# Performance work log

Measured on AMD Instinct MI355X. Metric: run time of the kernel, lower is better.

The kernel has to match this reference:

```python
import jax, jax.numpy as jnp
import numpy as np

N_ATOMS = 50000
N_INT = 800000  # interactions (i,j pairs)
N_IN = 128
NFM = 128
LOG2 = float(np.log(2.0))


def ssp(a):
    # shifted softplus: log(0.5*exp(x) + 0.5) = softplus(x) - log(2)
    return jax.nn.softplus(a) - LOG2


def setup_inputs() -> dict:
    key = jax.random.key(0)
    ks = jax.random.split(key, 12)
    s = 1.0 / np.sqrt(NFM)
    inp = {
        "x": jax.random.normal(ks[0], (N_ATOMS, NFM), dtype=jnp.float32),
        "dijk": jax.random.normal(ks[1], (N_INT, N_IN), dtype=jnp.float32),
        "idx_j": jax.random.randint(ks[2], (N_INT,), 0, N_ATOMS),
        "seg_i": jnp.sort(jax.random.randint(ks[3], (N_INT,), 0, N_ATOMS)),
        "seg_j": jnp.arange(N_INT),
        "seg_i_sum": jnp.ones((N_ATOMS,), dtype=jnp.int64 if jax.config.jax_enable_x64 else jnp.int32),
        # filternet params
        "W_f1": jax.random.normal(ks[4], (N_IN, NFM), dtype=jnp.float32) * s,
        "b_f1": jnp.zeros((NFM,), dtype=jnp.float32),
        "W_f2": jax.random.normal(ks[5], (NFM, NFM), dtype=jnp.float32) * s,
        "b_f2": jnp.zeros((NFM,), dtype=jnp.float32),
        # cfconv params
        "W_in2fac": jax.random.normal(ks[6], (NFM, NFM), dtype=jnp.float32) * s,
        "W_fac2out": jax.random.normal(ks[7], (NFM, NFM), dtype=jnp.float32) * s,
        "b_fac2out": jnp.zeros((NFM,), dtype=jnp.float32),
        # output dense params
        "W_dense": jax.random.normal(ks[8], (NFM, NFM), dtype=jnp.float32) * s,
        "b_dense": jnp.zeros((NFM,), dtype=jnp.float32),
    }
    return inp


def reference(x, dijk, idx_j, seg_i, seg_j, seg_i_sum,
              W_f1, b_f1, W_f2, b_f2,
              W_in2fac, W_fac2out, b_fac2out,
              W_dense, b_dense):
    n_atoms = x.shape[0]
    n_int = idx_j.shape[0]
    # CFnetFilter: two shifted-softplus dense layers over triples, pool -> per-interaction filters
    h = ssp(dijk @ W_f1 + b_f1)                                   # [T, nFM]
    w_ijk = ssp(h @ W_f2 + b_f2)                                  # [T, nFM]
    w_ij = jax.ops.segment_sum(w_ijk, seg_j, num_segments=n_int)  # [E, nFM]
    # CFConv: in2fac dense, gather neighbor features, filter-multiply, segment-sum pool, fac2out dense
    f = x @ W_in2fac                                              # [N, nFM]
    f_j = f[idx_j]                                                # gather -> [E, nFM]
    wf = w_ij * f_j                                               # [E, nFM]
    conv = jax.ops.segment_sum(wf, seg_i, num_segments=n_atoms)   # [N, nFM]
    c = ssp(conv @ W_fac2out + b_fac2out)                         # [N, nFM]
    # output dense (no activation) + residual
    v = c @ W_dense + b_dense                                     # [N, nFM]
    y = x + v
    return (y, v)
```

## Files before the change

kernel.cpp:

```cpp
#include <hip/hip_runtime.h>
#include <hip/hip_bf16.h>
#include <stdint.h>

#define NATOMS 50000
#define NINT   800000
#define NFM    128
#define VOFF   (NATOMS*NFM)
#define NBLK   (NINT/256)
#define CVROWS 512
#define CVBLK  ((NINT + CVROWS - 1)/CVROWS)

typedef __bf16 bf16x8 __attribute__((ext_vector_type(8)));
typedef float  f32x4  __attribute__((ext_vector_type(4)));
typedef unsigned short u16;
typedef u16 u16x8 __attribute__((ext_vector_type(8)));
typedef u16 u16x4 __attribute__((ext_vector_type(4)));

__device__ __forceinline__ u16 f2b(float f){
  __bf16 h = (__bf16)f;
  return __builtin_bit_cast(u16, h);
}
__device__ __forceinline__ float b2f(u16 v){
  return (float)__builtin_bit_cast(__bf16, v);
}

__device__ __forceinline__ float sspf(float x){
  float t = exp2f(x * 1.44269504088896f);
  return 0.69314718055995f * (log2f(1.0f + t) - 1.0f);
}

__global__ void zero_k(float4* __restrict__ p, int n4){
  int i = blockIdx.x * blockDim.x + threadIdx.x;
  int stride = gridDim.x * blockDim.x;
  float4 z = make_float4(0.f, 0.f, 0.f, 0.f);
  for (; i < n4; i += stride) p[i] = z;
}

__global__ void prep_weights_k(const float* __restrict__ w0, const float* __restrict__ w1,
                               const float* __restrict__ w2, const float* __restrict__ w3,
                               const float* __restrict__ w4, u16* __restrict__ wt){
  const float* srcs[5] = {w0, w1, w2, w3, w4};
  const float* src = srcs[blockIdx.x];
  u16* dst = wt + (size_t)blockIdx.x * NFM * NFM;
  for (int i = threadIdx.x; i < NFM*NFM; i += blockDim.x){
    int n = i >> 7, k = i & 127;
    dst[i] = f2b(src[k*NFM + n]);
  }
}

__device__ __forceinline__ void stage_inp(u16* lsA, const float* __restrict__ src,
                                          int base_row, int n_total, int t){
  #pragma unroll
  for (int pp = 0; pp < 8; ++pp){
    int id  = pp*512 + t;
    int row = id >> 4, c = id & 15;
    int grow = base_row + row;
    float4 v0 = make_float4(0.f,0.f,0.f,0.f), v1 = v0;
    if (grow < n_total){
      const float4* gp = reinterpret_cast<const float4*>(src + (size_t)grow*NFM + c*8);
      v0 = gp[0]; v1 = gp[1];
    }
    u16x8 pk;
    pk[0]=f2b(v0.x); pk[1]=f2b(v0.y); pk[2]=f2b(v0.z); pk[3]=f2b(v0.w);
    pk[4]=f2b(v1.x); pk[5]=f2b(v1.y); pk[6]=f2b(v1.z); pk[7]=f2b(v1.w);
    int byte = row*256 + ((c*16) ^ ((row & 7) << 4));
    *reinterpret_cast<u16x8*>(reinterpret_cast<char*>(lsA) + byte) = pk;
  }
}

__device__ __forceinline__ void stage_w(u16* lsW, const u16* __restrict__ wt, int t){
  #pragma unroll
  for (int pp = 0; pp < 4; ++pp){
    int id = pp*512 + t;
    int n = id >> 4, c = id & 15;
    u16x8 v = *reinterpret_cast<const u16x8*>(wt + n*NFM + c*8);
    int byte = n*256 + ((c*16) ^ ((n & 7) << 4));
    *reinterpret_cast<u16x8*>(reinterpret_cast<char*>(lsW) + byte) = v;
  }
}

__device__ __forceinline__ void gemm_tile(const u16* lsA, const u16* lsW,
                                          int wrow, int l15, int lk, f32x4 acc[2][8]){
  #pragma unroll
  for (int ks = 0; ks < 4; ++ks){
    int kb2 = (ks*32 + lk*8) * 2;
    int r0 = wrow + l15, r1 = wrow + 16 + l15;
    bf16x8 a0 = *reinterpret_cast<const bf16x8*>(reinterpret_cast<const char*>(lsA) + r0*256 + (kb2 ^ ((r0 & 7) << 4)));
    bf16x8 a1 = *reinterpret_cast<const bf16x8*>(reinterpret_cast<const char*>(lsA) + r1*256 + (kb2 ^ ((r1 & 7) << 4)));
    #pragma unroll
    for (int ni = 0; ni < 8; ++ni){
      int n = ni*16 + l15;
      bf16x8 b = *reinterpret_cast<const bf16x8*>(reinterpret_cast<const char*>(lsW) + n*256 + (kb2 ^ ((n & 7) << 4)));
      acc[0][ni] = __builtin_amdgcn_mfma_f32_16x16x32_bf16(a0, b, acc[0][ni], 0, 0, 0);
      acc[1][ni] = __builtin_amdgcn_mfma_f32_16x16x32_bf16(a1, b, acc[1][ni], 0, 0, 0);
    }
  }
}

__global__ __launch_bounds__(512, 2) void in2fac_k(const float* __restrict__ x,
                                                   const u16* __restrict__ wt,
                                                   u16* __restrict__ f_g){
  __shared__ u16 lsA[256*128];
  __shared__ u16 lsW[128*128];
  int t = threadIdx.x;
  int B0 = blockIdx.x * 256;
  stage_inp(lsA, x, B0, NATOMS, t);
  stage_w(lsW, wt, t);
  __syncthreads();
  int wid = t >> 6, lane = t & 63, l15 = lane & 15, lk = lane >> 4;
  int wrow = wid * 32;
  f32x4 acc[2][8] = {};
  gemm_tile(lsA, lsW, wrow, l15, lk, acc);
  #pragma unroll
  for (int mi = 0; mi < 2; ++mi)
    #pragma unroll
    for (int ni = 0; ni < 8; ++ni)
      #pragma unroll
      for (int j = 0; j < 4; ++j){
        int grow = B0 + wrow + mi*16 + lk*4 + j;
        if (grow < NATOMS) f_g[(size_t)grow*NFM + ni*16 + l15] = f2b(acc[mi][ni][j]);
      }
}

__global__ __launch_bounds__(512) __attribute__((amdgpu_waves_per_eu(4, 4)))
void filter_k(const float* __restrict__ dijk,
              const float* __restrict__ b_f1, const float* __restrict__ b_f2,
              const u16* __restrict__ wt1, const u16* __restrict__ wt2,
              u16* __restrict__ w_g){
  __shared__ u16 lsW[2*128*128];
  __shared__ u16 lsS[8192];
  int t = threadIdx.x;
  int B0 = blockIdx.x * 256;
  int wid = t >> 6, lane = t & 63, l15 = lane & 15, lk = lane >> 4;

  f32x4 araw[16];
  {
    const float* abase = dijk + (size_t)(B0 + wid*32 + l15) * NFM;
    #pragma unroll
    for (int mi = 0; mi < 2; ++mi)
      #pragma unroll
      for (int ks = 0; ks < 4; ++ks){
        const f32x4* gp = reinterpret_cast<const f32x4*>(abase + mi*16*NFM + ks*32 + lk*8);
        araw[(mi*4+ks)*2+0] = __builtin_nontemporal_load(gp);
        araw[(mi*4+ks)*2+1] = __builtin_nontemporal_load(gp+1);
      }
  }

  stage_w(lsW, wt1, t);
  stage_w(lsW + 16384, wt2, t);

  float bias1[8], bias2[8];
  #pragma unroll
  for (int ni = 0; ni < 8; ++ni){ bias1[ni] = b_f1[ni*16 + l15]; bias2[ni] = b_f2[ni*16 + l15]; }

  bf16x8 aa[2][4];
  #pragma unroll
  for (int mi = 0; mi < 2; ++mi)
    #pragma unroll
    for (int ks = 0; ks < 4; ++ks){
      f32x4 v0 = araw[(mi*4+ks)*2], v1 = araw[(mi*4+ks)*2+1];
      u16x8 pk;
      pk[0]=f2b(v0[0]); pk[1]=f2b(v0[1]); pk[2]=f2b(v0[2]); pk[3]=f2b(v0[3]);
      pk[4]=f2b(v1[0]); pk[5]=f2b(v1[1]); pk[6]=f2b(v1[2]); pk[7]=f2b(v1[3]);
      aa[mi][ks] = __builtin_bit_cast(bf16x8, pk);
    }

  __syncthreads();

  char* wbase = reinterpret_cast<char*>(lsS) + wid*2048;
  const char* lsW1b = reinterpret_cast<const char*>(lsW);
  const char* lsW2b = reinterpret_cast<const char*>(lsW + 16384);

  #pragma unroll
  for (int mi = 0; mi < 2; ++mi){
    f32x4 acc[8] = {};
    #pragma unroll
    for (int ks = 0; ks < 4; ++ks){
      int kb2 = (ks*32 + lk*8) * 2;
      #pragma unroll
      for (int ni = 0; ni < 8; ++ni){
        int n = ni*16 + l15;
        bf16x8 b = *reinterpret_cast<const bf16x8*>(lsW1b + n*256 + (kb2 ^ ((n & 7) << 4)));
        acc[ni] = __builtin_amdgcn_mfma_f32_16x16x32_bf16(aa[mi][ks], b, acc[ni], 0, 0, 0);
      }
    }
    bf16x8 h[4];
    #pragma unroll
    for (int p = 0; p < 2; ++p){
      #pragma unroll
      for (int nn = 0; nn < 4; ++nn){
        int col = nn*16 + l15;
        #pragma unroll
        for (int j = 0; j < 4; ++j){
          int r = lk*4 + j;
          *reinterpret_cast<u16*>(wbase + r*128 + ((col*2) ^ ((r & 7) << 4))) = f2b(sspf(acc[p*4+nn][j] + bias1[p*4+nn]));
        }
      }
      #pragma unroll
      for (int ksl = 0; ksl < 2; ++ksl)
        h[p*2+ksl] = *reinterpret_cast<const bf16x8*>(wbase + l15*128 + ((ksl*64 + lk*16) ^ ((l15 & 7) << 4)));
    }
    #pragma unroll
    for (int p = 0; p < 2; ++p){
      f32x4 acc2[4] = {};
      #pragma unroll
      for (int ks = 0; ks < 4; ++ks){
        int kb2 = (ks*32 + lk*8) * 2;
        #pragma unroll
        for (int nn = 0; nn < 4; ++nn){
          int n = (p*4 + nn)*16 + l15;
          bf16x8 b = *reinterpret_cast<const bf16x8*>(lsW2b + n*256 + (kb2 ^ ((n & 7) << 4)));
          acc2[nn] = __builtin_amdgcn_mfma_f32_16x16x32_bf16(h[ks], b, acc2[nn], 0, 0, 0);
        }
      }
      #pragma unroll
      for (int nn = 0; nn < 4; ++nn){
        int col = nn*16 + l15;
        #pragma unroll
        for (int j = 0; j < 4; ++j){
          int r = lk*4 + j;
          *reinterpret_cast<u16*>(wbase + r*128 + ((col*2) ^ ((r & 7) << 4))) = f2b(sspf(acc2[nn][j] + bias2[p*4+nn]));
        }
      }
      int row16 = lane & 15, chunk = lane >> 4;
      u16x8 v0 = *reinterpret_cast<const u16x8*>(wbase + row16*128 + ((chunk*32) ^ ((row16 & 7) << 4)));
      u16x8 v1 = *reinterpret_cast<const u16x8*>(wbase + row16*128 + ((chunk*32 + 16) ^ ((row16 & 7) << 4)));
      u16* gdst = w_g + (size_t)(B0 + wid*32 + mi*16 + row16)*NFM + p*64 + chunk*16;
      *reinterpret_cast<u16x8*>(gdst)     = v0;
      *reinterpret_cast<u16x8*>(gdst + 8) = v1;
    }
  }
}

__global__ __launch_bounds__(512) void conv_k(const int* __restrict__ idx_j,
    const int* __restrict__ seg_i, const u16* __restrict__ f_g,
    const u16* __restrict__ w_g, float* __restrict__ conv){
  __shared__ int lsSeg[CVROWS];
  __shared__ int lsIdx[CVROWS];
  int t = threadIdx.x;
  int B0 = blockIdx.x * CVROWS;
  int navail = NINT - B0; if (navail > CVROWS) navail = CVROWS;
  if (t < navail){ lsSeg[t] = seg_i[B0 + t]; lsIdx[t] = idx_j[B0 + t]; }
  __syncthreads();
  int col = t & 127, q = t >> 7;
  int qs = q*128;
  if (qs >= navail) return;
  int qe = qs + 128; if (qe > navail) qe = navail;
  int prevseg = (qs > 0) ? lsSeg[qs-1] : (B0 > 0 ? seg_i[B0-1] : -1);
  int nextseg = (qe < navail) ? lsSeg[qe] : (B0 + qe < NINT ? seg_i[B0+qe] : -1);
  const u16* wtile = w_g + (size_t)B0*NFM;
  float s = 0.f;
  int cur = lsSeg[qs], rs = qs;
  for (int base = qs; base < qe; base += 16){
    float wbuf[16], fbuf[16];
    #pragma unroll
    for (int k = 0; k < 16; ++k){
      int r = base + k;
      wbuf[k] = b2f(wtile[(size_t)r*NFM + col]);
      fbuf[k] = b2f(f_g[(size_t)lsIdx[r]*NFM + col]);
    }
    #pragma unroll
    for (int k = 0; k < 16; ++k){
      int r = base + k;
      int sg = lsSeg[r];
      if (sg != cur){
        float* dp = conv + (size_t)cur*NFM + col;
        if (rs == qs && prevseg == cur) atomicAdd(dp, s); else *dp = s;
        cur = sg; rs = r; s = 0.f;
      }
      s = fmaf(wbuf[k], fbuf[k], s);
    }
  }
  float* dp = conv + (size_t)cur*NFM + col;
  if ((rs == qs && prevseg == cur) || nextseg == cur) atomicAdd(dp, s); else *dp = s;
}

__global__ __launch_bounds__(512, 2) void out_k(const float* __restrict__ conv,
    const float* __restrict__ x, const u16* __restrict__ wt3, const u16* __restrict__ wt4,
    const float* __restrict__ b3, const float* __restrict__ b4, float* __restrict__ out){
  __shared__ u16 lsA[256*128];
  __shared__ u16 lsW1[128*128];
  __shared__ u16 lsW2[128*128];
  int t = threadIdx.x;
  int B0 = blockIdx.x * 256;
  stage_inp(lsA, conv, B0, NATOMS, t);
  stage_w(lsW1, wt3, t);
  stage_w(lsW2, wt4, t);
  __syncthreads();
  int wid = t >> 6, lane = t & 63, l15 = lane & 15, lk = lane >> 4;
  int wrow = wid * 32;
  float bias3[8], bias4[8];
  #pragma unroll
  for (int ni = 0; ni < 8; ++ni){ bias3[ni] = b3[ni*16 + l15]; bias4[ni] = b4[ni*16 + l15]; }

  f32x4 acc1[2][8] = {};
  gemm_tile(lsA, lsW1, wrow, l15, lk, acc1);
  #pragma unroll
  for (int mi = 0; mi < 2; ++mi)
    #pragma unroll
    for (int ni = 0; ni < 8; ++ni)
      #pragma unroll
      for (int j = 0; j < 4; ++j){
        int row = wrow + mi*16 + lk*4 + j;
        int col = ni*16 + l15;
        u16 hb = f2b(sspf(acc1[mi][ni][j] + bias3[ni]));
        int byte = row*256 + ((col*2) ^ ((row & 7) << 4));
        *reinterpret_cast<u16*>(reinterpret_cast<char*>(lsA) + byte) = hb;
      }

  f32x4 acc2[2][8] = {};
  gemm_tile(lsA, lsW2, wrow, l15, lk, acc2);
  #pragma unroll
  for (int mi = 0; mi < 2; ++mi)
    #pragma unroll
    for (int ni = 0; ni < 8; ++ni)
      #pragma unroll
      for (int j = 0; j < 4; ++j){
        int grow = B0 + wrow + mi*16 + lk*4 + j;
        if (grow < NATOMS){
          int col = ni*16 + l15;
          float v = acc2[mi][ni][j] + bias4[ni];
          float yv = x[(size_t)grow*NFM + col] + v;
          out[(size_t)grow*NFM + col] = yv;
          out[(size_t)VOFF + (size_t)grow*NFM + col] = v;
        }
      }
}

extern "C" void kernel_launch(void* const* d_in, const int* in_sizes, int n_in,
                              void* d_out, int out_size, void* d_ws, size_t ws_size,
                              hipStream_t stream){
  const float* x        = (const float*)d_in[0];
  const float* dijk     = (const float*)d_in[1];
  const int*   idx_j    = (const int*)d_in[2];
  const int*   seg_i    = (const int*)d_in[3];
  const float* W_f1     = (const float*)d_in[6];
  const float* b_f1     = (const float*)d_in[7];
  const float* W_f2     = (const float*)d_in[8];
  const float* b_f2     = (const float*)d_in[9];
  const float* W_in2fac = (const float*)d_in[10];
  const float* W_fac2o  = (const float*)d_in[11];
  const float* b_fac2o  = (const float*)d_in[12];
  const float* W_dense  = (const float*)d_in[13];
  const float* b_dense  = (const float*)d_in[14];
  float* out = (float*)d_out;

  char* ws = (char*)d_ws;
  u16*   f_g  = (u16*)ws;
  float* conv = (float*)(ws + 12800000);
  u16*   wt   = (u16*)(ws + 38400000);
  u16*   w_g  = (u16*)(ws + 38600000);
  u16* wt1 = wt;
  u16* wt2 = wt + 16384;
  u16* wt5 = wt + 2*16384;
  u16* wt3 = wt + 3*16384;
  u16* wt4 = wt + 4*16384;

  prep_weights_k<<<5, 256, 0, stream>>>(W_f1, W_f2, W_in2fac, W_fac2o, W_dense, wt);
  zero_k<<<2048, 256, 0, stream>>>(reinterpret_cast<float4*>(conv), NATOMS*NFM/4);
  in2fac_k<<<(NATOMS + 255)/256, 512, 0, stream>>>(x, wt5, f_g);
  filter_k<<<NBLK, 512, 0, stream>>>(dijk, b_f1, b_f2, wt1, wt2, w_g);
  conv_k<<<CVBLK, 512, 0, stream>>>(idx_j, seg_i, f_g, w_g, conv);
  out_k<<<(NATOMS + 255)/256, 512, 0, stream>>>(conv, x, wt3, wt4, b_fac2o, b_dense, out);
}
```

Baseline: 303.1 us.

## Split filter and conv into two chunks to keep filter output cache-resident

Runs the filter and conv kernels in two row chunks, each writing and then reading a half-sized w_g buffer at offset zero. The intent is for the filter output to still be in the large last-level cache when conv reads it, cutting HBM round-trip traffic. The conv kernel gains per-row guards because a chunk can end partway through a 16-row group. The cost is two extra kernel launches, slightly more branching in conv, and a reduced-occupancy tail for each chunk.

```diff
diff --git a/kernel.cpp b/kernel.cpp
--- a/kernel.cpp
+++ b/kernel.cpp
@@ -6,15 +6,18 @@
 #define NINT   800000
 #define NFM    128
 #define VOFF   (NATOMS*NFM)
-#define NBLK   (NINT/256)
+#define F0BLK  1563
+#define F1BLK  1562
+#define C0ROWS (F0BLK*256)
+#define C1ROWS (F1BLK*256)
 #define CVROWS 512
-#define CVBLK  ((NINT + CVROWS - 1)/CVROWS)
+#define CV0BLK ((C0ROWS + CVROWS - 1)/CVROWS)
+#define CV1BLK ((C1ROWS + CVROWS - 1)/CVROWS)
 
 typedef __bf16 bf16x8 __attribute__((ext_vector_type(8)));
 typedef float  f32x4  __attribute__((ext_vector_type(4)));
 typedef unsigned short u16;
 typedef u16 u16x8 __attribute__((ext_vector_type(8)));
-typedef u16 u16x4 __attribute__((ext_vector_type(4)));
 
 __device__ __forceinline__ u16 f2b(float f){
   __bf16 h = (__bf16)f;
@@ -126,11 +129,11 @@
 void filter_k(const float* __restrict__ dijk,
               const float* __restrict__ b_f1, const float* __restrict__ b_f2,
               const u16* __restrict__ wt1, const u16* __restrict__ wt2,
-              u16* __restrict__ w_g){
+              u16* __restrict__ w_g, int C0){
   __shared__ u16 lsW[2*128*128];
   __shared__ u16 lsS[8192];
   int t = threadIdx.x;
-  int B0 = blockIdx.x * 256;
+  int B0 = C0 + blockIdx.x * 256;
   int wid = t >> 6, lane = t & 63, l15 = lane & 15, lk = lane >> 4;
 
   f32x4 araw[16];
@@ -225,7 +228,7 @@
       int row16 = lane & 15, chunk = lane >> 4;
       u16x8 v0 = *reinterpret_cast<const u16x8*>(wbase + row16*128 + ((chunk*32) ^ ((row16 & 7) << 4)));
       u16x8 v1 = *reinterpret_cast<const u16x8*>(wbase + row16*128 + ((chunk*32 + 16) ^ ((row16 & 7) << 4)));
-      u16* gdst = w_g + (size_t)(B0 + wid*32 + mi*16 + row16)*NFM + p*64 + chunk*16;
+      u16* gdst = w_g + (size_t)(blockIdx.x*256 + wid*32 + mi*16 + row16)*NFM + p*64 + chunk*16;
       *reinterpret_cast<u16x8*>(gdst)     = v0;
       *reinterpret_cast<u16x8*>(gdst + 8) = v1;
     }
@@ -234,12 +237,13 @@
 
 __global__ __launch_bounds__(512) void conv_k(const int* __restrict__ idx_j,
     const int* __restrict__ seg_i, const u16* __restrict__ f_g,
-    const u16* __restrict__ w_g, float* __restrict__ conv){
+    const u16* __restrict__ w_g, float* __restrict__ conv, int C0, int NROWS){
   __shared__ int lsSeg[CVROWS];
   __shared__ int lsIdx[CVROWS];
   int t = threadIdx.x;
-  int B0 = blockIdx.x * CVROWS;
-  int navail = NINT - B0; if (navail > CVROWS) navail = CVROWS;
+  int L0 = blockIdx.x * CVROWS;
+  int B0 = C0 + L0;
+  int navail = NROWS - L0; if (navail > CVROWS) navail = CVROWS;
   if (t < navail){ lsSeg[t] = seg_i[B0 + t]; lsIdx[t] = idx_j[B0 + t]; }
   __syncthreads();
   int col = t & 127, q = t >> 7;
@@ -248,27 +252,32 @@
   int qe = qs + 128; if (qe > navail) qe = navail;
   int prevseg = (qs > 0) ? lsSeg[qs-1] : (B0 > 0 ? seg_i[B0-1] : -1);
   int nextseg = (qe < navail) ? lsSeg[qe] : (B0 + qe < NINT ? seg_i[B0+qe] : -1);
-  const u16* wtile = w_g + (size_t)B0*NFM;
+  const u16* wtile = w_g + (size_t)L0*NFM;
   float s = 0.f;
   int cur = lsSeg[qs], rs = qs;
   for (int base = qs; base < qe; base += 16){
+    int bend = base + 16; if (bend > qe) bend = qe;
     float wbuf[16], fbuf[16];
     #pragma unroll
     for (int k = 0; k < 16; ++k){
       int r = base + k;
-      wbuf[k] = b2f(wtile[(size_t)r*NFM + col]);
-      fbuf[k] = b2f(f_g[(size_t)lsIdx[r]*NFM + col]);
+      if (r < bend){
+        wbuf[k] = b2f(wtile[(size_t)r*NFM + col]);
+        fbuf[k] = b2f(f_g[(size_t)lsIdx[r]*NFM + col]);
+      } else { wbuf[k] = 0.f; fbuf[k] = 0.f; }
     }
     #pragma unroll
     for (int k = 0; k < 16; ++k){
       int r = base + k;
-      int sg = lsSeg[r];
-      if (sg != cur){
-        float* dp = conv + (size_t)cur*NFM + col;
-        if (rs == qs && prevseg == cur) atomicAdd(dp, s); else *dp = s;
-        cur = sg; rs = r; s = 0.f;
-      }
-      s = fmaf(wbuf[k], fbuf[k], s);
+      if (r < bend){
+        int sg = lsSeg[r];
+        if (sg != cur){
+          float* dp = conv + (size_t)cur*NFM + col;
+          if (rs == qs && prevseg == cur) atomicAdd(dp, s); else *dp = s;
+          cur = sg; rs = r; s = 0.f;
+        }
+        s = fmaf(wbuf[k], fbuf[k], s);
+      }
     }
   }
   float* dp = conv + (size_t)cur*NFM + col;
@@ -359,7 +368,9 @@
   prep_weights_k<<<5, 256, 0, stream>>>(W_f1, W_f2, W_in2fac, W_fac2o, W_dense, wt);
   zero_k<<<2048, 256, 0, stream>>>(reinterpret_cast<float4*>(conv), NATOMS*NFM/4);
   in2fac_k<<<(NATOMS + 255)/256, 512, 0, stream>>>(x, wt5, f_g);
-  filter_k<<<NBLK, 512, 0, stream>>>(dijk, b_f1, b_f2, wt1, wt2, w_g);
-  conv_k<<<CVBLK, 512, 0, stream>>>(idx_j, seg_i, f_g, w_g, conv);
+  filter_k<<<F0BLK, 512, 0, stream>>>(dijk, b_f1, b_f2, wt1, wt2, w_g, 0);
+  conv_k<<<CV0BLK, 512, 0, stream>>>(idx_j, seg_i, f_g, w_g, conv, 0, C0ROWS);
+  filter_k<<<F1BLK, 512, 0, stream>>>(dijk, b_f1, b_f2, wt1, wt2, w_g, C0ROWS);
+  conv_k<<<CV1BLK, 512, 0, stream>>>(idx_j, seg_i, f_g, w_g, conv, C0ROWS, C1ROWS);
   out_k<<<(NATOMS + 255)/256, 512, 0, stream>>>(conv, x, wt3, wt4, b_fac2o, b_dense, out);
 }
```

New measurement: 447.2 us. 47.6% more time.
